# Kernel optimization log

Measured on AMD Instinct MI355X. Metric: run time of the kernel, lower is better.

The kernel has to match this reference:

```python
import jax, jax.numpy as jnp
import numpy as np

N = 50000      # num nodes
E = 800000     # num edges
IN_C = 256
OUT_C = 128


def setup_inputs() -> dict:
    key = jax.random.key(0)
    k1, k2, k3, k4 = jax.random.split(key, 4)
    x = jax.random.normal(k1, (N, IN_C), dtype=jnp.float32)
    edge_index = jax.random.randint(k2, (2, E), 0, N, dtype=jnp.int64)
    # Linear params (Kaiming-uniform-ish scale like torch Linear reset)
    bound = 1.0 / np.sqrt(IN_C)
    W = jax.random.uniform(k3, (OUT_C, IN_C), minval=-bound, maxval=bound, dtype=jnp.float32)
    b = jax.random.uniform(k4, (OUT_C,), minval=-bound, maxval=bound, dtype=jnp.float32)
    return {"x": x, "edge_index": edge_index, "W": W, "b": b}


def reference(x, edge_index, W, b):
    # out = Linear(x): [N, OUT_C]
    out = jnp.einsum("ni,oi->no", x, W) + b
    src, dst = edge_index[0], edge_index[1]
    # gather source features: [E, OUT_C]
    src_feat = out[src]
    # scatter-mean by destination node
    summed = jax.ops.segment_sum(src_feat, dst, num_segments=N)  # [N, OUT_C]
    counts = jax.ops.segment_sum(jnp.ones((E,), dtype=out.dtype), dst, num_segments=N)
    mean = summed / jnp.maximum(counts, 1.0)[:, None]
    return mean
```

## Files before the change

### kernel.cpp

```cpp
#include <hip/hip_runtime.h>

#define N_NODES 50000
#define N_EDGES 800000
#define IN_CH   256
#define OUT_CH  128

#define NB        391
#define CAP       3072
#define L1_CHUNK  2048
#define L1_BLOCKS ((N_EDGES + L1_CHUNK - 1) / L1_CHUNK)

typedef __attribute__((ext_vector_type(8))) short short8;
typedef __attribute__((ext_vector_type(4))) float f32x4;

__device__ __forceinline__ short f2bf(float f) {
    unsigned u = __float_as_uint(f);
    unsigned r = (u + 0x7fffu + ((u >> 16) & 1u)) >> 16;
    return (short)r;
}

#define GBM 128
#define GBK 32
#define LDK 40
__global__ __launch_bounds__(256) void gemm_mfma(const float* __restrict__ x,
                                                 const float* __restrict__ W,
                                                 const float* __restrict__ bias,
                                                 short* __restrict__ linbf) {
    __shared__ short As[GBM * LDK];
    __shared__ short Bs[OUT_CH * LDK];

    const int tid = threadIdx.x;
    const int m0  = blockIdx.x * GBM;
    const int w    = tid >> 6;
    const int lane = tid & 63;
    const int lm   = lane & 15;
    const int lq   = lane >> 4;
    const int wrow = (w >> 1) * 64;
    const int wcol = (w & 1) * 64;

    f32x4 acc[4][4];
#pragma unroll
    for (int i = 0; i < 4; ++i)
#pragma unroll
        for (int j = 0; j < 4; ++j) acc[i][j] = (f32x4)(0.0f);

    const int srow  = tid >> 1;
    const int shalf = tid & 1;

    for (int k0 = 0; k0 < IN_CH; k0 += GBK) {
        {
            float4 v0 = make_float4(0.f,0.f,0.f,0.f), v1 = v0, v2 = v0, v3 = v0;
            if (m0 + srow < N_NODES) {
                const float* xp = x + (size_t)(m0 + srow) * IN_CH + k0 + shalf * 16;
                v0 = ((const float4*)xp)[0];
                v1 = ((const float4*)xp)[1];
                v2 = ((const float4*)xp)[2];
                v3 = ((const float4*)xp)[3];
            }
            short8 s0, s1;
            s0[0]=f2bf(v0.x); s0[1]=f2bf(v0.y); s0[2]=f2bf(v0.z); s0[3]=f2bf(v0.w);
            s0[4]=f2bf(v1.x); s0[5]=f2bf(v1.y); s0[6]=f2bf(v1.z); s0[7]=f2bf(v1.w);
            s1[0]=f2bf(v2.x); s1[1]=f2bf(v2.y); s1[2]=f2bf(v2.z); s1[3]=f2bf(v2.w);
            s1[4]=f2bf(v3.x); s1[5]=f2bf(v3.y); s1[6]=f2bf(v3.z); s1[7]=f2bf(v3.w);
            *(short8*)&As[srow * LDK + shalf * 16]     = s0;
            *(short8*)&As[srow * LDK + shalf * 16 + 8] = s1;
        }
        {
            const float* wp = W + (size_t)srow * IN_CH + k0 + shalf * 16;
            float4 v0 = ((const float4*)wp)[0];
            float4 v1 = ((const float4*)wp)[1];
            float4 v2 = ((const float4*)wp)[2];
            float4 v3 = ((const float4*)wp)[3];
            short8 s0, s1;
            s0[0]=f2bf(v0.x); s0[1]=f2bf(v0.y); s0[2]=f2bf(v0.z); s0[3]=f2bf(v0.w);
            s0[4]=f2bf(v1.x); s0[5]=f2bf(v1.y); s0[6]=f2bf(v1.z); s0[7]=f2bf(v1.w);
            s1[0]=f2bf(v2.x); s1[1]=f2bf(v2.y); s1[2]=f2bf(v2.z); s1[3]=f2bf(v2.w);
            s1[4]=f2bf(v3.x); s1[5]=f2bf(v3.y); s1[6]=f2bf(v3.z); s1[7]=f2bf(v3.w);
            *(short8*)&Bs[srow * LDK + shalf * 16]     = s0;
            *(short8*)&Bs[srow * LDK + shalf * 16 + 8] = s1;
        }
        __syncthreads();

        short8 af[4], bfr[4];
#pragma unroll
        for (int rt = 0; rt < 4; ++rt)
            af[rt] = *(const short8*)&As[(wrow + rt * 16 + lm) * LDK + lq * 8];
#pragma unroll
        for (int ct = 0; ct < 4; ++ct)
            bfr[ct] = *(const short8*)&Bs[(wcol + ct * 16 + lm) * LDK + lq * 8];
#pragma unroll
        for (int rt = 0; rt < 4; ++rt)
#pragma unroll
            for (int ct = 0; ct < 4; ++ct)
                acc[rt][ct] = __builtin_amdgcn_mfma_f32_16x16x32_bf16(
                    af[rt], bfr[ct], acc[rt][ct], 0, 0, 0);
        __syncthreads();
    }

#pragma unroll
    for (int ct = 0; ct < 4; ++ct) {
        int gcol = wcol + ct * 16 + lm;
        float bv = bias[gcol];
#pragma unroll
        for (int rt = 0; rt < 4; ++rt) {
#pragma unroll
            for (int r = 0; r < 4; ++r) {
                int grow = m0 + wrow + rt * 16 + lq * 4 + r;
                if (grow < N_NODES)
                    linbf[(size_t)grow * OUT_CH + gcol] = f2bf(acc[rt][ct][r] + bv);
            }
        }
    }
}

__global__ __launch_bounds__(256) void bucket_scatter(const int* __restrict__ src,
                                                      const int* __restrict__ dst,
                                                      int* __restrict__ bcnt,
                                                      uint2* __restrict__ rec) {
    __shared__ int  lhist[NB];
    __shared__ int  lscan[NB];
    __shared__ int  lbase[NB];
    __shared__ uint2 staged[L1_CHUNK];

    const int tid = threadIdx.x;
    const int e0  = blockIdx.x * L1_CHUNK;
    const int total = min(L1_CHUNK, N_EDGES - e0);

    for (int i = tid; i < NB; i += 256) lhist[i] = 0;
    __syncthreads();

    int myd[8], mys[8], myr[8];
#pragma unroll
    for (int j = 0; j < 8; ++j) {
        int i = tid + j * 256;
        myd[j] = -1;
        if (i < total) {
            int d = dst[e0 + i];
            int s = src[e0 + i];
            myd[j] = d; mys[j] = s;
            myr[j] = atomicAdd(&lhist[d >> 7], 1);
        }
    }
    __syncthreads();

    if (tid < 64) {
        int carry = 0;
        for (int c = 0; c < NB; c += 64) {
            int idx = c + tid;
            int v = (idx < NB) ? lhist[idx] : 0;
            int incl = v;
#pragma unroll
            for (int s = 1; s < 64; s <<= 1) {
                int t = __shfl_up(incl, s, 64);
                if (tid >= s) incl += t;
            }
            if (idx < NB) lscan[idx] = carry + incl - v;
            carry += __shfl(incl, 63, 64);
        }
    }
    __syncthreads();

    for (int bkt = tid; bkt < NB; bkt += 256) {
        int c = lhist[bkt];
        lbase[bkt] = c ? atomicAdd(&bcnt[bkt], c) : 0;
    }
#pragma unroll
    for (int j = 0; j < 8; ++j) {
        if (myd[j] >= 0) {
            int b = myd[j] >> 7;
            staged[lscan[b] + myr[j]] = make_uint2((unsigned)mys[j], (unsigned)myd[j]);
        }
    }
    __syncthreads();

    for (int p = tid; p < total; p += 256) {
        uint2 r = staged[p];
        int b = (int)(r.y >> 7);
        int gpos = lbase[b] + (p - lscan[b]);
        if (gpos < CAP)
            rec[(size_t)b * CAP + gpos] = r;
    }
}

__global__ __launch_bounds__(256) void fine_sort(const int* __restrict__ bcnt,
                                                 const uint2* __restrict__ rec,
                                                 int* __restrict__ srcs,
                                                 int* __restrict__ off_g,
                                                 int* __restrict__ deg_g) {
    __shared__ int sdst[CAP];
    __shared__ int ssrc[CAP];
    __shared__ int fh[128], fo[128], fc[128];

    const int b = blockIdx.x;
    const int tid = threadIdx.x;
    const int cnt = min(bcnt[b], CAP);

    for (int i = tid; i < cnt; i += 256) {
        uint2 r = rec[(size_t)b * CAP + i];
        sdst[i] = (int)(r.y & 127u);
        ssrc[i] = (int)r.x;
    }
    if (tid < 128) fh[tid] = 0;
    __syncthreads();

    for (int i = tid; i < cnt; i += 256) atomicAdd(&fh[sdst[i]], 1);
    __syncthreads();

    if (tid < 64) {
        int carry = 0;
        for (int c = 0; c < 128; c += 64) {
            int v = fh[c + tid];
            int incl = v;
#pragma unroll
            for (int s = 1; s < 64; s <<= 1) {
                int t = __shfl_up(incl, s, 64);
                if (tid >= s) incl += t;
            }
            fo[c + tid] = carry + incl - v;
            carry += __shfl(incl, 63, 64);
        }
    }
    __syncthreads();

    if (tid < 128) {
        int node = b * 128 + tid;
        if (node < N_NODES) {
            off_g[node] = b * (CAP * 2) + fo[tid];
            deg_g[node] = fh[tid];
        }
        fc[tid] = fo[tid];
    }
    __syncthreads();

    for (int i = tid; i < cnt; i += 256) {
        int r = atomicAdd(&fc[sdst[i]], 1);
        srcs[(size_t)b * (CAP * 2) + r] = ssrc[i];
    }
}

__global__ __launch_bounds__(256) void gather_mean(const int* __restrict__ srcs,
                                                   const int* __restrict__ off_g,
                                                   const int* __restrict__ deg_g,
                                                   const short* __restrict__ linbf,
                                                   float* __restrict__ out) {
    int n = blockIdx.x * 16 + (threadIdx.x >> 4);
    if (n >= N_NODES) return;
    const int l = threadIdx.x & 15;
    const int beg = off_g[n];
    const int deg = deg_g[n];
    const int end = beg + deg;

    float a[8];
#pragma unroll
    for (int j = 0; j < 8; ++j) a[j] = 0.0f;

    int i = beg;
    for (; i + 1 < end; i += 2) {
        int s0 = srcs[i];
        int s1 = srcs[i + 1];
        uint4 u0 = *(const uint4*)&linbf[(size_t)s0 * OUT_CH + l * 8];
        uint4 u1 = *(const uint4*)&linbf[(size_t)s1 * OUT_CH + l * 8];
        const unsigned* p0 = (const unsigned*)&u0;
        const unsigned* p1 = (const unsigned*)&u1;
#pragma unroll
        for (int j = 0; j < 4; ++j) {
            a[2*j]   += __uint_as_float(p0[j] << 16) + __uint_as_float(p1[j] << 16);
            a[2*j+1] += __uint_as_float(p0[j] & 0xffff0000u) + __uint_as_float(p1[j] & 0xffff0000u);
        }
    }
    if (i < end) {
        int s0 = srcs[i];
        uint4 u0 = *(const uint4*)&linbf[(size_t)s0 * OUT_CH + l * 8];
        const unsigned* p0 = (const unsigned*)&u0;
#pragma unroll
        for (int j = 0; j < 4; ++j) {
            a[2*j]   += __uint_as_float(p0[j] << 16);
            a[2*j+1] += __uint_as_float(p0[j] & 0xffff0000u);
        }
    }
    float inv = 1.0f / (float)(deg > 1 ? deg : 1);
    float4 o0, o1;
    o0.x = a[0]*inv; o0.y = a[1]*inv; o0.z = a[2]*inv; o0.w = a[3]*inv;
    o1.x = a[4]*inv; o1.y = a[5]*inv; o1.z = a[6]*inv; o1.w = a[7]*inv;
    float* op = &out[(size_t)n * OUT_CH + l * 8];
    ((float4*)op)[0] = o0;
    ((float4*)op)[1] = o1;
}

extern "C" void kernel_launch(void* const* d_in, const int* in_sizes, int n_in,
                              void* d_out, int out_size, void* d_ws, size_t ws_size,
                              hipStream_t stream) {
    const float* x  = (const float*)d_in[0];
    const int*   ei = (const int*)d_in[1];
    const float* W  = (const float*)d_in[2];
    const float* b  = (const float*)d_in[3];
    float* out = (float*)d_out;

    const int* src = ei;
    const int* dst = ei + N_EDGES;

    char* ws = (char*)d_ws;
    short* linbf = (short*)ws;  ws += ((size_t)N_NODES * OUT_CH * sizeof(short) + 255) & ~255ull;
    uint2* rec   = (uint2*)ws;  ws += ((size_t)NB * CAP * sizeof(uint2) + 255) & ~255ull;
    int*   off_g = (int*)ws;    ws += ((size_t)N_NODES * sizeof(int) + 255) & ~255ull;
    int*   deg_g = (int*)ws;    ws += ((size_t)N_NODES * sizeof(int) + 255) & ~255ull;
    int*   bcnt  = (int*)ws;
    int*   srcs  = (int*)rec;

    hipMemsetAsync(bcnt, 0, (size_t)NB * sizeof(int), stream);

    gemm_mfma<<<(N_NODES + GBM - 1) / GBM, 256, 0, stream>>>(x, W, b, linbf);
    bucket_scatter<<<L1_BLOCKS, 256, 0, stream>>>(src, dst, bcnt, rec);
    fine_sort<<<NB, 256, 0, stream>>>(bcnt, rec, srcs, off_g, deg_g);
    gather_mean<<<(N_NODES + 15) / 16, 256, 0, stream>>>(srcs, off_g, deg_g, linbf, out);
}
```

Before: 173.6 us.

## Pack edge records to 32 bits, use 16-bit sources, prebake bf16 W

Edge records are packed into one 32-bit word (16-bit source, 7-bit local destination, 9-bit bucket id), and the sorted source list is stored as 16-bit indices. This halves the bytes moved through the bucket and fine-sort stages and through the gather index reads. A small kernel converts W to bf16 once and zeroes the bucket counters, replacing the memset, so GEMM blocks no longer redo the W conversion. The gather loop is also unrolled to four edges to keep more loads in flight. The packing depends on N < 65536 and fewer than 512 buckets, which holds for the fixed sizes here.

```diff
diff --git a/kernel.cpp b/kernel.cpp
--- a/kernel.cpp
+++ b/kernel.cpp
@@ -19,11 +19,25 @@
     return (short)r;
 }
 
+__global__ __launch_bounds__(256) void convert_w(const float* __restrict__ W,
+                                                 short* __restrict__ Wbf,
+                                                 int* __restrict__ bcnt) {
+    int t = blockIdx.x * 256 + threadIdx.x;
+    const float* wp = W + t * 8;
+    float4 v0 = ((const float4*)wp)[0];
+    float4 v1 = ((const float4*)wp)[1];
+    short8 s;
+    s[0]=f2bf(v0.x); s[1]=f2bf(v0.y); s[2]=f2bf(v0.z); s[3]=f2bf(v0.w);
+    s[4]=f2bf(v1.x); s[5]=f2bf(v1.y); s[6]=f2bf(v1.z); s[7]=f2bf(v1.w);
+    *(short8*)&Wbf[t * 8] = s;
+    if (t < NB) bcnt[t] = 0;
+}
+
 #define GBM 128
 #define GBK 32
 #define LDK 40
 __global__ __launch_bounds__(256) void gemm_mfma(const float* __restrict__ x,
-                                                 const float* __restrict__ W,
+                                                 const short* __restrict__ Wbf,
                                                  const float* __restrict__ bias,
                                                  short* __restrict__ linbf) {
     __shared__ short As[GBM * LDK];
@@ -66,18 +80,9 @@
             *(short8*)&As[srow * LDK + shalf * 16 + 8] = s1;
         }
         {
-            const float* wp = W + (size_t)srow * IN_CH + k0 + shalf * 16;
-            float4 v0 = ((const float4*)wp)[0];
-            float4 v1 = ((const float4*)wp)[1];
-            float4 v2 = ((const float4*)wp)[2];
-            float4 v3 = ((const float4*)wp)[3];
-            short8 s0, s1;
-            s0[0]=f2bf(v0.x); s0[1]=f2bf(v0.y); s0[2]=f2bf(v0.z); s0[3]=f2bf(v0.w);
-            s0[4]=f2bf(v1.x); s0[5]=f2bf(v1.y); s0[6]=f2bf(v1.z); s0[7]=f2bf(v1.w);
-            s1[0]=f2bf(v2.x); s1[1]=f2bf(v2.y); s1[2]=f2bf(v2.z); s1[3]=f2bf(v2.w);
-            s1[4]=f2bf(v3.x); s1[5]=f2bf(v3.y); s1[6]=f2bf(v3.z); s1[7]=f2bf(v3.w);
-            *(short8*)&Bs[srow * LDK + shalf * 16]     = s0;
-            *(short8*)&Bs[srow * LDK + shalf * 16 + 8] = s1;
+            const short* wp = Wbf + (size_t)srow * IN_CH + k0 + shalf * 16;
+            *(short8*)&Bs[srow * LDK + shalf * 16]     = ((const short8*)wp)[0];
+            *(short8*)&Bs[srow * LDK + shalf * 16 + 8] = ((const short8*)wp)[1];
         }
         __syncthreads();
 
@@ -116,11 +121,11 @@
 __global__ __launch_bounds__(256) void bucket_scatter(const int* __restrict__ src,
                                                       const int* __restrict__ dst,
                                                       int* __restrict__ bcnt,
-                                                      uint2* __restrict__ rec) {
-    __shared__ int  lhist[NB];
-    __shared__ int  lscan[NB];
-    __shared__ int  lbase[NB];
-    __shared__ uint2 staged[L1_CHUNK];
+                                                      unsigned* __restrict__ rec) {
+    __shared__ int lhist[NB];
+    __shared__ int lscan[NB];
+    __shared__ int lbase[NB];
+    __shared__ unsigned staged[L1_CHUNK];
 
     const int tid = threadIdx.x;
     const int e0  = blockIdx.x * L1_CHUNK;
@@ -129,16 +134,20 @@
     for (int i = tid; i < NB; i += 256) lhist[i] = 0;
     __syncthreads();
 
-    int myd[8], mys[8], myr[8];
+    unsigned mypk[8];
+    int myr[8];
+    int myb[8];
 #pragma unroll
     for (int j = 0; j < 8; ++j) {
         int i = tid + j * 256;
-        myd[j] = -1;
+        myb[j] = -1;
         if (i < total) {
-            int d = dst[e0 + i];
-            int s = src[e0 + i];
-            myd[j] = d; mys[j] = s;
-            myr[j] = atomicAdd(&lhist[d >> 7], 1);
+            unsigned d = (unsigned)dst[e0 + i];
+            unsigned s = (unsigned)src[e0 + i];
+            int b = (int)(d >> 7);
+            myb[j] = b;
+            mypk[j] = s | ((d & 127u) << 16) | ((unsigned)b << 23);
+            myr[j] = atomicAdd(&lhist[b], 1);
         }
     }
     __syncthreads();
@@ -166,16 +175,14 @@
     }
 #pragma unroll
     for (int j = 0; j < 8; ++j) {
-        if (myd[j] >= 0) {
-            int b = myd[j] >> 7;
-            staged[lscan[b] + myr[j]] = make_uint2((unsigned)mys[j], (unsigned)myd[j]);
-        }
+        if (myb[j] >= 0)
+            staged[lscan[myb[j]] + myr[j]] = mypk[j];
     }
     __syncthreads();
 
     for (int p = tid; p < total; p += 256) {
-        uint2 r = staged[p];
-        int b = (int)(r.y >> 7);
+        unsigned r = staged[p];
+        int b = (int)(r >> 23);
         int gpos = lbase[b] + (p - lscan[b]);
         if (gpos < CAP)
             rec[(size_t)b * CAP + gpos] = r;
@@ -183,27 +190,24 @@
 }
 
 __global__ __launch_bounds__(256) void fine_sort(const int* __restrict__ bcnt,
-                                                 const uint2* __restrict__ rec,
-                                                 int* __restrict__ srcs,
+                                                 const unsigned* __restrict__ rec,
+                                                 unsigned short* __restrict__ srcs,
                                                  int* __restrict__ off_g,
                                                  int* __restrict__ deg_g) {
-    __shared__ int sdst[CAP];
-    __shared__ int ssrc[CAP];
+    __shared__ unsigned srec[CAP];
     __shared__ int fh[128], fo[128], fc[128];
 
     const int b = blockIdx.x;
     const int tid = threadIdx.x;
     const int cnt = min(bcnt[b], CAP);
 
-    for (int i = tid; i < cnt; i += 256) {
-        uint2 r = rec[(size_t)b * CAP + i];
-        sdst[i] = (int)(r.y & 127u);
-        ssrc[i] = (int)r.x;
-    }
+    for (int i = tid; i < cnt; i += 256)
+        srec[i] = rec[(size_t)b * CAP + i];
     if (tid < 128) fh[tid] = 0;
     __syncthreads();
 
-    for (int i = tid; i < cnt; i += 256) atomicAdd(&fh[sdst[i]], 1);
+    for (int i = tid; i < cnt; i += 256)
+        atomicAdd(&fh[(srec[i] >> 16) & 127u], 1);
     __syncthreads();
 
     if (tid < 64) {
@@ -225,7 +229,7 @@
     if (tid < 128) {
         int node = b * 128 + tid;
         if (node < N_NODES) {
-            off_g[node] = b * (CAP * 2) + fo[tid];
+            off_g[node] = b * CAP + fo[tid];
             deg_g[node] = fh[tid];
         }
         fc[tid] = fo[tid];
@@ -233,12 +237,13 @@
     __syncthreads();
 
     for (int i = tid; i < cnt; i += 256) {
-        int r = atomicAdd(&fc[sdst[i]], 1);
-        srcs[(size_t)b * (CAP * 2) + r] = ssrc[i];
-    }
-}
-
-__global__ __launch_bounds__(256) void gather_mean(const int* __restrict__ srcs,
+        unsigned r = srec[i];
+        int p = atomicAdd(&fc[(r >> 16) & 127u], 1);
+        srcs[(size_t)b * CAP + p] = (unsigned short)(r & 0xffffu);
+    }
+}
+
+__global__ __launch_bounds__(256) void gather_mean(const unsigned short* __restrict__ srcs,
                                                    const int* __restrict__ off_g,
                                                    const int* __restrict__ deg_g,
                                                    const short* __restrict__ linbf,
@@ -255,22 +260,26 @@
     for (int j = 0; j < 8; ++j) a[j] = 0.0f;
 
     int i = beg;
-    for (; i + 1 < end; i += 2) {
-        int s0 = srcs[i];
-        int s1 = srcs[i + 1];
-        uint4 u0 = *(const uint4*)&linbf[(size_t)s0 * OUT_CH + l * 8];
-        uint4 u1 = *(const uint4*)&linbf[(size_t)s1 * OUT_CH + l * 8];
-        const unsigned* p0 = (const unsigned*)&u0;
-        const unsigned* p1 = (const unsigned*)&u1;
-#pragma unroll
-        for (int j = 0; j < 4; ++j) {
-            a[2*j]   += __uint_as_float(p0[j] << 16) + __uint_as_float(p1[j] << 16);
-            a[2*j+1] += __uint_as_float(p0[j] & 0xffff0000u) + __uint_as_float(p1[j] & 0xffff0000u);
-        }
-    }
-    if (i < end) {
-        int s0 = srcs[i];
-        uint4 u0 = *(const uint4*)&linbf[(size_t)s0 * OUT_CH + l * 8];
+    for (; i + 3 < end; i += 4) {
+        uint4 u[4];
+#pragma unroll
+        for (int e = 0; e < 4; ++e) {
+            int s = srcs[i + e];
+            u[e] = *(const uint4*)&linbf[(size_t)s * OUT_CH + l * 8];
+        }
+#pragma unroll
+        for (int e = 0; e < 4; ++e) {
+            const unsigned* p = (const unsigned*)&u[e];
+#pragma unroll
+            for (int j = 0; j < 4; ++j) {
+                a[2*j]   += __uint_as_float(p[j] << 16);
+                a[2*j+1] += __uint_as_float(p[j] & 0xffff0000u);
+            }
+        }
+    }
+    for (; i < end; ++i) {
+        int s = srcs[i];
+        uint4 u0 = *(const uint4*)&linbf[(size_t)s * OUT_CH + l * 8];
         const unsigned* p0 = (const unsigned*)&u0;
 #pragma unroll
         for (int j = 0; j < 4; ++j) {
@@ -300,16 +309,17 @@
     const int* dst = ei + N_EDGES;
 
     char* ws = (char*)d_ws;
-    short* linbf = (short*)ws;  ws += ((size_t)N_NODES * OUT_CH * sizeof(short) + 255) & ~255ull;
-    uint2* rec   = (uint2*)ws;  ws += ((size_t)NB * CAP * sizeof(uint2) + 255) & ~255ull;
-    int*   off_g = (int*)ws;    ws += ((size_t)N_NODES * sizeof(int) + 255) & ~255ull;
-    int*   deg_g = (int*)ws;    ws += ((size_t)N_NODES * sizeof(int) + 255) & ~255ull;
-    int*   bcnt  = (int*)ws;
-    int*   srcs  = (int*)rec;
-
-    hipMemsetAsync(bcnt, 0, (size_t)NB * sizeof(int), stream);
-
-    gemm_mfma<<<(N_NODES + GBM - 1) / GBM, 256, 0, stream>>>(x, W, b, linbf);
+    short*    linbf = (short*)ws;    ws += ((size_t)N_NODES * OUT_CH * sizeof(short) + 255) & ~255ull;
+    short*    Wbf   = (short*)ws;    ws += ((size_t)IN_CH * OUT_CH * sizeof(short) + 255) & ~255ull;
+    unsigned* rec   = (unsigned*)ws; ws += ((size_t)NB * CAP * sizeof(unsigned) + 255) & ~255ull;
+    unsigned short* srcs = (unsigned short*)ws;
+                                     ws += ((size_t)NB * CAP * sizeof(unsigned short) + 255) & ~255ull;
+    int* off_g = (int*)ws;           ws += ((size_t)N_NODES * sizeof(int) + 255) & ~255ull;
+    int* deg_g = (int*)ws;           ws += ((size_t)N_NODES * sizeof(int) + 255) & ~255ull;
+    int* bcnt  = (int*)ws;
+
+    convert_w<<<16, 256, 0, stream>>>(W, Wbf, bcnt);
+    gemm_mfma<<<(N_NODES + GBM - 1) / GBM, 256, 0, stream>>>(x, Wbf, b, linbf);
     bucket_scatter<<<L1_BLOCKS, 256, 0, stream>>>(src, dst, bcnt, rec);
     fine_sort<<<NB, 256, 0, stream>>>(bcnt, rec, srcs, off_g, deg_g);
     gather_mean<<<(N_NODES + 15) / 16, 256, 0, stream>>>(srcs, off_g, deg_g, linbf, out);
```

Measured after the change: 163.3 us. 1.06x faster.
